# Performance work log

Measured on AMD Instinct MI355X. Metric: run time of the kernel, lower is better.

Reference implementation:

```python
import jax, jax.numpy as jnp
import numpy as np

EMBED_DIM = 1024
NUM_HEADS = 16
HEAD_DIM = EMBED_DIM // NUM_HEADS


def setup_inputs() -> dict:
    key = jax.random.key(0)
    ks = jax.random.split(key, 9)
    s = 1.0 / np.sqrt(EMBED_DIM)
    x = jax.random.normal(ks[0], (4, 2048, EMBED_DIM), dtype=jnp.float32)
    # torch.nn.Linear weights are [out_features, in_features]
    Wq = jax.random.uniform(ks[1], (EMBED_DIM, EMBED_DIM), jnp.float32, -s, s)
    bq = jax.random.uniform(ks[2], (EMBED_DIM,), jnp.float32, -s, s)
    Wk = jax.random.uniform(ks[3], (EMBED_DIM, EMBED_DIM), jnp.float32, -s, s)
    bk = jax.random.uniform(ks[4], (EMBED_DIM,), jnp.float32, -s, s)
    Wv = jax.random.uniform(ks[5], (EMBED_DIM, EMBED_DIM), jnp.float32, -s, s)
    bv = jax.random.uniform(ks[6], (EMBED_DIM,), jnp.float32, -s, s)
    Wo = jax.random.uniform(ks[7], (EMBED_DIM, EMBED_DIM), jnp.float32, -s, s)
    bo = jax.random.uniform(ks[8], (EMBED_DIM,), jnp.float32, -s, s)
    return {"x": x, "Wq": Wq, "bq": bq, "Wk": Wk, "bk": bk,
            "Wv": Wv, "bv": bv, "Wo": Wo, "bo": bo}


def reference(x, Wq, bq, Wk, bk, Wv, bv, Wo, bo):
    B, S, E = x.shape
    H, D = NUM_HEADS, HEAD_DIM

    def proj(W, b):
        y = jnp.einsum('bse,fe->bsf', x, W) + b          # Linear: x @ W.T + b
        return y.reshape(B, S, H, D).transpose(0, 2, 1, 3)  # [B,H,S,D]

    q = proj(Wq, bq)
    k = proj(Wk, bk)
    v = proj(Wv, bv)

    scores = jnp.einsum('bhqd,bhkd->bhqk', q, k) / jnp.sqrt(jnp.float32(D))
    attn = jax.nn.soft_sign(scores)                      # softsign, no normalization
    # dropout p=0.0 -> identity
    ctx = jnp.einsum('bhqk,bhkd->bhqd', attn, v)         # [B,H,S,D]
    ctx = ctx.transpose(0, 2, 1, 3).reshape(B, S, E)
    out = jnp.einsum('bse,fe->bsf', ctx, Wo) + bo
    return (out,)
```

## Files before the change

### kernel.cpp

```cpp
#include <hip/hip_runtime.h>
#include <hip/hip_bf16.h>
#include <stdint.h>

#define Bb 4
#define SEQ 2048
#define Ee 1024
#define Hh 16
#define Dh 64
#define Mm (Bb*SEQ)

typedef __attribute__((ext_vector_type(8))) short bfrag;
typedef __attribute__((ext_vector_type(4))) float f32x4;
typedef unsigned short u16;

__device__ __forceinline__ u16 f2bf(float x) {
  __hip_bfloat16 h = __float2bfloat16(x);
  return *reinterpret_cast<u16*>(&h);
}

__device__ __forceinline__ void gll16(const void* g, void* l) {
  __builtin_amdgcn_global_load_lds(
      (const __attribute__((address_space(1))) void*)g,
      (__attribute__((address_space(3))) void*)l, 16, 0, 0);
}

__global__ __launch_bounds__(256) void cast_all(
    const float* __restrict__ x,  const float* __restrict__ wq,
    const float* __restrict__ wk, const float* __restrict__ wv,
    const float* __restrict__ wo,
    u16* __restrict__ xb, u16* __restrict__ wqb, u16* __restrict__ wkb,
    u16* __restrict__ wvb, u16* __restrict__ wob)
{
  int idx = blockIdx.x * 256 + threadIdx.x;
  const float* src; u16* dst; int off;
  if (idx < 2097152) { src = x; dst = xb; off = idx; }
  else {
    int t = idx - 2097152;
    int seg = t >> 18;
    off = t & 262143;
    src = (seg == 0) ? wq : (seg == 1) ? wk : (seg == 2) ? wv : wo;
    dst = (seg == 0) ? wqb : (seg == 1) ? wkb : (seg == 2) ? wvb : wob;
  }
  float4 v = reinterpret_cast<const float4*>(src)[off];
  ushort4 o;
  o.x = f2bf(v.x); o.y = f2bf(v.y); o.z = f2bf(v.z); o.w = f2bf(v.w);
  reinterpret_cast<ushort4*>(dst)[off] = o;
}

template<int OUTMODE>
__global__ __launch_bounds__(256) void gemm_bt(
    const u16* __restrict__ A,
    const u16* __restrict__ W0, const u16* __restrict__ W1, const u16* __restrict__ W2,
    const float* __restrict__ b0, const float* __restrict__ b1, const float* __restrict__ b2,
    void* __restrict__ outp, int K, int N)
{
  __shared__ __align__(16) u16 smem[16384];
  u16* As = smem;
  u16* Bs = smem + 8192;
  const int tid  = threadIdx.x;
  const int lane = tid & 63;
  const int wid  = tid >> 6;
  const int bm = blockIdx.x * 128;
  const int bn = blockIdx.y * 128;
  const int z  = blockIdx.z;
  const u16*  Wp = (z == 0) ? W0 : (z == 1) ? W1 : W2;
  const float* bp = (z == 0) ? b0 : (z == 1) ? b1 : b2;
  const int wr = (wid >> 1) * 64, wc = (wid & 1) * 64;
  const int lr = lane & 15, lk = (lane >> 4) * 8;
  f32x4 acc[4][4] = {};

  for (int kt = 0; kt < K; kt += 64) {
    __syncthreads();
#pragma unroll
    for (int p = 0; p < 4; ++p) {
      int flat = p * 2048 + tid * 8;
      int r = flat >> 6, c = flat & 63;
      gll16(A + (size_t)(bm + r) * K + kt + c, As + flat);
    }
#pragma unroll
    for (int p = 0; p < 4; ++p) {
      int flat = p * 2048 + tid * 8;
      int r = flat >> 6, c = flat & 63;
      gll16(Wp + (size_t)(bn + r) * K + kt + c, Bs + flat);
    }
    __syncthreads();
#pragma unroll
    for (int kk = 0; kk < 2; ++kk) {
      bfrag a[4], b[4];
#pragma unroll
      for (int i = 0; i < 4; ++i)
        a[i] = *reinterpret_cast<const bfrag*>(&As[(wr + i * 16 + lr) * 64 + kk * 32 + lk]);
#pragma unroll
      for (int j = 0; j < 4; ++j)
        b[j] = *reinterpret_cast<const bfrag*>(&Bs[(wc + j * 16 + lr) * 64 + kk * 32 + lk]);
#pragma unroll
      for (int i = 0; i < 4; ++i)
#pragma unroll
        for (int j = 0; j < 4; ++j)
          acc[i][j] = __builtin_amdgcn_mfma_f32_16x16x32_bf16(a[i], b[j], acc[i][j], 0, 0, 0);
    }
  }

  float bias[4];
#pragma unroll
  for (int j = 0; j < 4; ++j) bias[j] = bp[bn + wc + j * 16 + (lane & 15)];

  if (OUTMODE == 0) {
    __syncthreads();
    u16* cst = smem;
#pragma unroll
    for (int i = 0; i < 4; ++i)
#pragma unroll
      for (int j = 0; j < 4; ++j)
#pragma unroll
        for (int e = 0; e < 4; ++e)
          cst[(wr + i * 16 + (lane >> 4) * 4 + e) * 128 + wc + j * 16 + (lane & 15)] =
              f2bf(acc[i][j][e] + bias[j]);
    __syncthreads();
    u16* outb = (u16*)outp + (size_t)z * (size_t)Mm * Ee;
#pragma unroll
    for (int p = 0; p < 8; ++p) {
      int chunk = p * 256 + tid;
      int r = chunk >> 4;
      int c = (chunk & 15) * 8;
      int m = bm + r, f = bn + c;
      u16* dst = outb + ((((size_t)(m >> 11) * Hh + (f >> 6)) * SEQ + (m & 2047)) * Dh + (f & 63));
      *reinterpret_cast<bfrag*>(dst) = *reinterpret_cast<const bfrag*>(&cst[r * 128 + c]);
    }
  } else {
    float* outf = (float*)outp;
    float* cf = reinterpret_cast<float*>(smem);
#pragma unroll
    for (int half = 0; half < 2; ++half) {
      __syncthreads();
      if ((wid >> 1) == half) {
#pragma unroll
        for (int i = 0; i < 4; ++i)
#pragma unroll
          for (int j = 0; j < 4; ++j)
#pragma unroll
            for (int e = 0; e < 4; ++e)
              cf[(i * 16 + (lane >> 4) * 4 + e) * 128 + wc + j * 16 + (lane & 15)] =
                  acc[i][j][e] + bias[j];
      }
      __syncthreads();
#pragma unroll
      for (int p = 0; p < 8; ++p) {
        int chunk = p * 256 + tid;
        int r = chunk >> 5;
        int c = (chunk & 31) * 4;
        *reinterpret_cast<float4*>(&outf[(size_t)(bm + half * 64 + r) * N + bn + c]) =
            *reinterpret_cast<const float4*>(&cf[r * 128 + c]);
      }
    }
  }
}

__global__ __launch_bounds__(256) void transpose_v(const u16* __restrict__ v,
                                                   u16* __restrict__ vt)
{
  __shared__ __align__(16) u16 lds[8192];
  const int tid = threadIdx.x;
  const int bh = blockIdx.y;
  const int st = blockIdx.x * 128;
  const u16* vb = v + (size_t)bh * SEQ * Dh;
#pragma unroll
  for (int p = 0; p < 4; ++p) {
    int flat = p * 2048 + tid * 8;
    int s = flat >> 6, dp = flat & 63;
    int dl = dp ^ (((s >> 3) & 7) << 3);
    gll16(vb + (size_t)(st + s) * Dh + dl, lds + flat);
  }
  __syncthreads();
  u16* vtb = vt + (size_t)bh * Dh * SEQ;
#pragma unroll
  for (int p = 0; p < 4; ++p) {
    int chunk = p * 256 + tid;
    int sc = chunk & 15, d = chunk >> 4;
    int X = (sc & 7) << 3;
    bfrag o;
#pragma unroll
    for (int e = 0; e < 8; ++e)
      o[e] = (short)lds[(sc * 8 + e) * 64 + (d ^ X)];
    *reinterpret_cast<bfrag*>(&vtb[(size_t)d * SEQ + st + sc * 8]) = o;
  }
}

__global__ __launch_bounds__(256) void attn_kernel(
    const u16* __restrict__ qg, const u16* __restrict__ kg,
    const u16* __restrict__ vtg, u16* __restrict__ ctx)
{
  __shared__ __align__(16) u16 smem[24576];
  const int tid  = threadIdx.x;
  const int lane = tid & 63;
  const int wid  = tid >> 6;
  const int lr = lane & 15, lk = (lane >> 4) * 8;
  const int g = lane >> 4, c = lane & 15;

  const int orig = blockIdx.y * 16 + blockIdx.x;
  const int swz  = (orig & 7) * 128 + (orig >> 3);
  const int q0 = (swz & 15) * 128;
  const int bh = swz >> 4;

  const u16* qb  = qg  + (size_t)bh * SEQ * Dh;
  const u16* kb  = kg  + (size_t)bh * SEQ * Dh;
  const u16* vtb = vtg + (size_t)bh * Dh * SEQ;
  u16* Pw = smem + 16384 + wid * 2048;

  bfrag aq[2][2];
#pragma unroll
  for (int mi = 0; mi < 2; ++mi)
#pragma unroll
    for (int kk = 0; kk < 2; ++kk)
      aq[mi][kk] = *reinterpret_cast<const bfrag*>(
          &qb[(size_t)(q0 + wid * 32 + mi * 16 + lr) * Dh + kk * 32 + lk]);

  f32x4 o[2][4] = {};

  auto stage = [&](int kt, int buf) {
#pragma unroll
    for (int p = 0; p < 2; ++p) {
      int flat = p * 2048 + tid * 8;
      int r = flat >> 6, cp = flat & 63;
      int cl = cp ^ ((r & 7) << 3);
      gll16(kb + (size_t)(kt + r) * Dh + cl, smem + buf * 4096 + flat);
    }
#pragma unroll
    for (int p = 0; p < 2; ++p) {
      int flat = p * 2048 + tid * 8;
      int r = flat >> 6, cp = flat & 63;
      int cl = cp ^ ((r & 7) << 3);
      gll16(vtb + (size_t)r * SEQ + kt + cl, smem + 8192 + buf * 4096 + flat);
    }
  };

  stage(0, 0);
  __syncthreads();

  for (int ti = 0; ti < 32; ++ti) {
    const int cur = ti & 1;
    if (ti < 31) stage((ti + 1) * 64, cur ^ 1);
    const u16* Kb = smem + cur * 4096;
    const u16* Vb = smem + 8192 + cur * 4096;

    f32x4 s[2][4] = {};
#pragma unroll
    for (int kk = 0; kk < 2; ++kk) {
      bfrag bk[4];
#pragma unroll
      for (int n = 0; n < 4; ++n) {
        int row = n * 16 + lr;
        bk[n] = *reinterpret_cast<const bfrag*>(
            &Kb[row * 64 + ((kk * 32 + lk) ^ ((row & 7) << 3))]);
      }
#pragma unroll
      for (int mi = 0; mi < 2; ++mi)
#pragma unroll
        for (int n = 0; n < 4; ++n)
          s[mi][n] = __builtin_amdgcn_mfma_f32_16x16x32_bf16(aq[mi][kk], bk[n], s[mi][n], 0, 0, 0);
    }

#pragma unroll
    for (int mi = 0; mi < 2; ++mi)
#pragma unroll
      for (int n = 0; n < 4; ++n)
#pragma unroll
        for (int e = 0; e < 4; ++e) {
          int prow = mi * 16 + g * 4 + e;
          float sv = s[mi][n][e];
          float pv = sv * __builtin_amdgcn_rcpf(8.0f + __builtin_fabsf(sv));
          Pw[prow * 64 + ((n * 16 + c) ^ ((prow & 7) << 3))] = f2bf(pv);
        }

#pragma unroll
    for (int kk = 0; kk < 2; ++kk) {
      bfrag ap[2], bv[4];
#pragma unroll
      for (int mi = 0; mi < 2; ++mi) {
        int row = mi * 16 + lr;
        ap[mi] = *reinterpret_cast<const bfrag*>(
            &Pw[row * 64 + ((kk * 32 + lk) ^ ((row & 7) << 3))]);
      }
#pragma unroll
      for (int n = 0; n < 4; ++n) {
        int row = n * 16 + lr;
        bv[n] = *reinterpret_cast<const bfrag*>(
            &Vb[row * 64 + ((kk * 32 + lk) ^ ((row & 7) << 3))]);
      }
#pragma unroll
      for (int mi = 0; mi < 2; ++mi)
#pragma unroll
        for (int n = 0; n < 4; ++n)
          o[mi][n] = __builtin_amdgcn_mfma_f32_16x16x32_bf16(ap[mi], bv[n], o[mi][n], 0, 0, 0);
    }
    __syncthreads();
  }

  u16* cst = smem;
#pragma unroll
  for (int mi = 0; mi < 2; ++mi)
#pragma unroll
    for (int n = 0; n < 4; ++n)
#pragma unroll
      for (int e = 0; e < 4; ++e)
        cst[(wid * 32 + mi * 16 + g * 4 + e) * 64 + n * 16 + c] = f2bf(o[mi][n][e]);
  __syncthreads();
  const int b = bh >> 4, h = bh & 15;
#pragma unroll
  for (int p = 0; p < 4; ++p) {
    int chunk = p * 256 + tid;
    int r = chunk >> 3, cc = (chunk & 7) * 8;
    u16* dst = ctx + ((size_t)(b * SEQ + q0 + r) * Ee + h * Dh + cc);
    *reinterpret_cast<bfrag*>(dst) = *reinterpret_cast<const bfrag*>(&cst[r * 64 + cc]);
  }
}

extern "C" void kernel_launch(void* const* d_in, const int* in_sizes, int n_in,
                              void* d_out, int out_size, void* d_ws, size_t ws_size,
                              hipStream_t stream)
{
  const float* x  = (const float*)d_in[0];
  const float* Wq = (const float*)d_in[1];
  const float* bq = (const float*)d_in[2];
  const float* Wk = (const float*)d_in[3];
  const float* bk = (const float*)d_in[4];
  const float* Wv = (const float*)d_in[5];
  const float* bv = (const float*)d_in[6];
  const float* Wo = (const float*)d_in[7];
  const float* bo = (const float*)d_in[8];
  float* out = (float*)d_out;

  u16* ws  = (u16*)d_ws;
  u16* xb  = ws;
  u16* wqb = ws + 8388608;
  u16* wkb = wqb + 1048576;
  u16* wvb = wkb + 1048576;
  u16* wob = wvb + 1048576;
  u16* qkv = wob + 1048576;
  u16* q_  = qkv;
  u16* k_  = qkv + 8388608;
  u16* v_  = qkv + 2 * 8388608;
  u16* vt  = xb;
  u16* ctx = v_;

  cast_all<<<12288, 256, 0, stream>>>(x, Wq, Wk, Wv, Wo, xb, wqb, wkb, wvb, wob);

  gemm_bt<0><<<dim3(64, 8, 3), 256, 0, stream>>>(xb, wqb, wkb, wvb, bq, bk, bv,
                                                 qkv, Ee, Ee);
  transpose_v<<<dim3(16, 64), 256, 0, stream>>>(v_, vt);
  attn_kernel<<<dim3(16, 64), 256, 0, stream>>>(q_, k_, vt, ctx);
  gemm_bt<1><<<dim3(64, 8, 1), 256, 0, stream>>>(ctx, wob, wob, wob, bo, bo, bo,
                                                 out, Ee, Ee);
}
```

Baseline: 316.8 us.

## Compute transposed scores with 32x32 MFMA and keep P in registers

The attention kernel now computes S^T = K·Q^T using 32x32x16 bf16 MFMAs, so the softsign output lands directly in the register layout needed as the A operand of the P·V MFMA. This removes the per-wave LDS round trip for the P tile and cuts LDS use. Each block now handles 256 queries instead of 128 over a 1D grid of 512 blocks, which doubles K/V reuse per staged tile. The V-transpose kernel permutes the sequence order within each 16-key group to match the new P register layout, so correctness depends on that permutation and the MFMA layouts lining up exactly.

```diff
diff --git a/kernel.cpp b/kernel.cpp
--- a/kernel.cpp
+++ b/kernel.cpp
@@ -11,6 +11,7 @@
 
 typedef __attribute__((ext_vector_type(8))) short bfrag;
 typedef __attribute__((ext_vector_type(4))) float f32x4;
+typedef __attribute__((ext_vector_type(16))) float f32x16;
 typedef unsigned short u16;
 
 __device__ __forceinline__ u16 f2bf(float x) {
@@ -177,45 +178,48 @@
   for (int p = 0; p < 4; ++p) {
     int chunk = p * 256 + tid;
     int sc = chunk & 15, d = chunk >> 4;
-    int X = (sc & 7) << 3;
     bfrag o;
 #pragma unroll
-    for (int e = 0; e < 8; ++e)
-      o[e] = (short)lds[(sc * 8 + e) * 64 + (d ^ X)];
+    for (int e = 0; e < 8; ++e) {
+      int sp = sc * 8 + e;
+      int ss = (sp & 0x63) | ((sp & 4) << 1) | ((sp & 8) >> 1) | (sp & 0x70);
+      ss = (sp & ~12) | ((sp & 4) << 1) | ((sp & 8) >> 1);
+      int X = ((ss >> 3) & 7) << 3;
+      o[e] = (short)lds[ss * 64 + (d ^ X)];
+    }
     *reinterpret_cast<bfrag*>(&vtb[(size_t)d * SEQ + st + sc * 8]) = o;
   }
 }
 
 __global__ __launch_bounds__(256) void attn_kernel(
-    const u16* __restrict__ qg, const u16* __restrict__ kg,
+    const u16* __restrict__ qg_, const u16* __restrict__ kg,
     const u16* __restrict__ vtg, u16* __restrict__ ctx)
 {
-  __shared__ __align__(16) u16 smem[24576];
+  __shared__ __align__(16) u16 smem[16384];
   const int tid  = threadIdx.x;
   const int lane = tid & 63;
   const int wid  = tid >> 6;
-  const int lr = lane & 15, lk = (lane >> 4) * 8;
-  const int g = lane >> 4, c = lane & 15;
-
-  const int orig = blockIdx.y * 16 + blockIdx.x;
-  const int swz  = (orig & 7) * 128 + (orig >> 3);
-  const int q0 = (swz & 15) * 128;
-  const int bh = swz >> 4;
-
-  const u16* qb  = qg  + (size_t)bh * SEQ * Dh;
+  const int ql = lane & 31;
+  const int hi = lane >> 5;
+
+  const int orig = blockIdx.x;
+  const int swz  = (orig & 7) * 64 + (orig >> 3);
+  const int bh = swz >> 3;
+  const int q0 = (swz & 7) * 256;
+
+  const u16* qb  = qg_ + (size_t)bh * SEQ * Dh;
   const u16* kb  = kg  + (size_t)bh * SEQ * Dh;
   const u16* vtb = vtg + (size_t)bh * Dh * SEQ;
-  u16* Pw = smem + 16384 + wid * 2048;
-
-  bfrag aq[2][2];
-#pragma unroll
-  for (int mi = 0; mi < 2; ++mi)
-#pragma unroll
-    for (int kk = 0; kk < 2; ++kk)
-      aq[mi][kk] = *reinterpret_cast<const bfrag*>(
-          &qb[(size_t)(q0 + wid * 32 + mi * 16 + lr) * Dh + kk * 32 + lk]);
-
-  f32x4 o[2][4] = {};
+
+  bfrag qf[2][4];
+#pragma unroll
+  for (int qg2 = 0; qg2 < 2; ++qg2)
+#pragma unroll
+    for (int db = 0; db < 4; ++db)
+      qf[qg2][db] = *reinterpret_cast<const bfrag*>(
+          &qb[(size_t)(q0 + wid * 64 + qg2 * 32 + ql) * Dh + db * 16 + hi * 8]);
+
+  f32x16 o[2][2] = {};
 
   auto stage = [&](int kt, int buf) {
 #pragma unroll
@@ -243,71 +247,55 @@
     const u16* Kb = smem + cur * 4096;
     const u16* Vb = smem + 8192 + cur * 4096;
 
-    f32x4 s[2][4] = {};
-#pragma unroll
-    for (int kk = 0; kk < 2; ++kk) {
-      bfrag bk[4];
-#pragma unroll
-      for (int n = 0; n < 4; ++n) {
-        int row = n * 16 + lr;
-        bk[n] = *reinterpret_cast<const bfrag*>(
-            &Kb[row * 64 + ((kk * 32 + lk) ^ ((row & 7) << 3))]);
+#pragma unroll
+    for (int kh = 0; kh < 2; ++kh) {
+      f32x16 s[2] = {};
+      const int krow = kh * 32 + ql;
+      const int ksw = (krow & 7) << 3;
+#pragma unroll
+      for (int db = 0; db < 4; ++db) {
+        bfrag ka = *reinterpret_cast<const bfrag*>(
+            &Kb[krow * 64 + ((db * 16 + hi * 8) ^ ksw)]);
+        s[0] = __builtin_amdgcn_mfma_f32_32x32x16_bf16(ka, qf[0][db], s[0], 0, 0, 0);
+        s[1] = __builtin_amdgcn_mfma_f32_32x32x16_bf16(ka, qf[1][db], s[1], 0, 0, 0);
       }
-#pragma unroll
-      for (int mi = 0; mi < 2; ++mi)
-#pragma unroll
-        for (int n = 0; n < 4; ++n)
-          s[mi][n] = __builtin_amdgcn_mfma_f32_16x16x32_bf16(aq[mi][kk], bk[n], s[mi][n], 0, 0, 0);
-    }
-
-#pragma unroll
-    for (int mi = 0; mi < 2; ++mi)
-#pragma unroll
-      for (int n = 0; n < 4; ++n)
-#pragma unroll
-        for (int e = 0; e < 4; ++e) {
-          int prow = mi * 16 + g * 4 + e;
-          float sv = s[mi][n][e];
+      bfrag pa[2][2];
+#pragma unroll
+      for (int qg2 = 0; qg2 < 2; ++qg2)
+#pragma unroll
+        for (int r = 0; r < 16; ++r) {
+          float sv = s[qg2][r];
           float pv = sv * __builtin_amdgcn_rcpf(8.0f + __builtin_fabsf(sv));
-          Pw[prow * 64 + ((n * 16 + c) ^ ((prow & 7) << 3))] = f2bf(pv);
+          pa[qg2][r >> 3][r & 7] = (short)f2bf(pv);
         }
-
-#pragma unroll
-    for (int kk = 0; kk < 2; ++kk) {
-      bfrag ap[2], bv[4];
-#pragma unroll
-      for (int mi = 0; mi < 2; ++mi) {
-        int row = mi * 16 + lr;
-        ap[mi] = *reinterpret_cast<const bfrag*>(
-            &Pw[row * 64 + ((kk * 32 + lk) ^ ((row & 7) << 3))]);
+#pragma unroll
+      for (int tt = 0; tt < 2; ++tt)
+#pragma unroll
+        for (int dh = 0; dh < 2; ++dh) {
+          const int vrow = dh * 32 + ql;
+          bfrag vb = *reinterpret_cast<const bfrag*>(
+              &Vb[vrow * 64 + ((kh * 32 + tt * 16 + hi * 8) ^ ((vrow & 7) << 3))]);
+          o[0][dh] = __builtin_amdgcn_mfma_f32_32x32x16_bf16(pa[0][tt], vb, o[0][dh], 0, 0, 0);
+          o[1][dh] = __builtin_amdgcn_mfma_f32_32x32x16_bf16(pa[1][tt], vb, o[1][dh], 0, 0, 0);
+        }
+    }
+    __syncthreads();
+  }
+
+  u16* cst = smem;
+#pragma unroll
+  for (int qg2 = 0; qg2 < 2; ++qg2)
+#pragma unroll
+    for (int dh = 0; dh < 2; ++dh)
+#pragma unroll
+      for (int r = 0; r < 16; ++r) {
+        int qrow = wid * 64 + qg2 * 32 + (r & 3) + 8 * (r >> 2) + 4 * hi;
+        cst[qrow * 64 + dh * 32 + ql] = f2bf(o[qg2][dh][r]);
       }
-#pragma unroll
-      for (int n = 0; n < 4; ++n) {
-        int row = n * 16 + lr;
-        bv[n] = *reinterpret_cast<const bfrag*>(
-            &Vb[row * 64 + ((kk * 32 + lk) ^ ((row & 7) << 3))]);
-      }
-#pragma unroll
-      for (int mi = 0; mi < 2; ++mi)
-#pragma unroll
-        for (int n = 0; n < 4; ++n)
-          o[mi][n] = __builtin_amdgcn_mfma_f32_16x16x32_bf16(ap[mi], bv[n], o[mi][n], 0, 0, 0);
-    }
-    __syncthreads();
-  }
-
-  u16* cst = smem;
-#pragma unroll
-  for (int mi = 0; mi < 2; ++mi)
-#pragma unroll
-    for (int n = 0; n < 4; ++n)
-#pragma unroll
-      for (int e = 0; e < 4; ++e)
-        cst[(wid * 32 + mi * 16 + g * 4 + e) * 64 + n * 16 + c] = f2bf(o[mi][n][e]);
   __syncthreads();
   const int b = bh >> 4, h = bh & 15;
 #pragma unroll
-  for (int p = 0; p < 4; ++p) {
+  for (int p = 0; p < 8; ++p) {
     int chunk = p * 256 + tid;
     int r = chunk >> 3, cc = (chunk & 7) * 8;
     u16* dst = ctx + ((size_t)(b * SEQ + q0 + r) * Ee + h * Dh + cc);
@@ -348,7 +336,7 @@
   gemm_bt<0><<<dim3(64, 8, 3), 256, 0, stream>>>(xb, wqb, wkb, wvb, bq, bk, bv,
                                                  qkv, Ee, Ee);
   transpose_v<<<dim3(16, 64), 256, 0, stream>>>(v_, vt);
-  attn_kernel<<<dim3(16, 64), 256, 0, stream>>>(q_, k_, vt, ctx);
+  attn_kernel<<<512, 256, 0, stream>>>(q_, k_, vt, ctx);
   gemm_bt<1><<<dim3(64, 8, 1), 256, 0, stream>>>(ctx, wob, wob, wob, bo, bo, bo,
                                                  out, Ee, Ee);
 }
```

Measured after the change: 305.4 us. 3.6% less time.
